# Kernel optimization log

Hardware: AMD Instinct MI355X
Metric: run time of the kernel (lower is better)

The kernel has to match this reference:

```python
import jax, jax.numpy as jnp
import numpy as np

B, T = 2, 4096
TOK_DIM, POS_DIM = 64, 64
N_HEADS, HEAD_DIM = 8, 32
D_MODEL = 256


def setup_inputs() -> dict:
    key = jax.random.key(0)
    ks = jax.random.split(key, 5)
    s = 0.02
    return {
        "x": jax.random.normal(ks[0], (B, T, TOK_DIM + POS_DIM), dtype=jnp.float32),
        "Wq": jax.random.normal(ks[1], (POS_DIM, N_HEADS * HEAD_DIM), dtype=jnp.float32) * s,
        "Wk": jax.random.normal(ks[2], (POS_DIM, N_HEADS * HEAD_DIM), dtype=jnp.float32) * s,
        "Wv": jax.random.normal(ks[3], (TOK_DIM, N_HEADS * HEAD_DIM), dtype=jnp.float32) * s,
        "Wo": jax.random.normal(ks[4], (N_HEADS * HEAD_DIM, D_MODEL), dtype=jnp.float32) * s,
    }


def reference(x, Wq, Wk, Wv, Wo):
    Bb, Tt, _ = x.shape
    x_tok = x[:, :, :TOK_DIM]   # V comes from token dims
    x_pos = x[:, :, TOK_DIM:]   # Q,K come from positional dims

    # [B, T, H, Dh] -> [B, H, T, Dh]
    q = (x_pos @ Wq).reshape(Bb, Tt, N_HEADS, HEAD_DIM).transpose(0, 2, 1, 3)
    k = (x_pos @ Wk).reshape(Bb, Tt, N_HEADS, HEAD_DIM).transpose(0, 2, 1, 3)
    v = (x_tok @ Wv).reshape(Bb, Tt, N_HEADS, HEAD_DIM).transpose(0, 2, 1, 3)

    scale = 1.0 / jnp.sqrt(jnp.float32(HEAD_DIM))
    scores = jnp.einsum("bhqd,bhkd->bhqk", q, k) * scale  # [B,H,T,T]
    causal = jnp.tril(jnp.ones((Tt, Tt), dtype=bool))
    scores = jnp.where(causal[None, None, :, :], scores, -jnp.inf)
    attn = jax.nn.softmax(scores, axis=-1)

    out = jnp.einsum("bhqk,bhkd->bhqd", attn, v)          # [B,H,T,Dh]
    out = out.transpose(0, 2, 1, 3).reshape(Bb, Tt, N_HEADS * HEAD_DIM)
    return out @ Wo
```

## Files before the change

### kernel.cpp

```cpp
#include <hip/hip_runtime.h>

typedef __attribute__((ext_vector_type(8))) short bf16x8;
typedef __attribute__((ext_vector_type(4))) float f32x4;
typedef __attribute__((ext_vector_type(16))) float f32x16;

#define NB 2
#define SEQ 4096
#define NHD 8
#define HDIM 32
#define DMODEL 256

#define QSCALE 0.25503506f

__device__ __forceinline__ short f2bf(float f) {
  union { float f; unsigned u; } v; v.f = f;
  unsigned r = v.u + 0x7fffu + ((v.u >> 16) & 1u);
  return (short)(r >> 16);
}

__global__ __launch_bounds__(256) void proj_kernel(
    const float* __restrict__ x, const float* __restrict__ Wq,
    const float* __restrict__ Wk, const float* __restrict__ Wv,
    short* __restrict__ Q, short* __restrict__ K, short* __restrict__ VT)
{
  __shared__ float xs[8][128];
  const int tid = threadIdx.x;
  const int row0 = blockIdx.x * 8;
  {
    const float4* src = (const float4*)(x + (size_t)row0 * 128);
    float4* dst = (float4*)xs;
    dst[tid] = src[tid];
  }
  __syncthreads();
  const int c = tid;
  float qa[8], ka[8], va[8];
#pragma unroll
  for (int r = 0; r < 8; ++r) { qa[r] = 0.f; ka[r] = 0.f; va[r] = 0.f; }
  for (int d4 = 0; d4 < 16; ++d4) {
    float wq[4], wk[4], wv[4];
#pragma unroll
    for (int j = 0; j < 4; ++j) {
      const int d = d4 * 4 + j;
      wq[j] = Wq[d * 256 + c];
      wk[j] = Wk[d * 256 + c];
      wv[j] = Wv[d * 256 + c];
    }
#pragma unroll
    for (int r = 0; r < 8; ++r) {
      const float4 xt = *(const float4*)&xs[r][d4 * 4];
      const float4 xp = *(const float4*)&xs[r][64 + d4 * 4];
      qa[r] += xp.x * wq[0] + xp.y * wq[1] + xp.z * wq[2] + xp.w * wq[3];
      ka[r] += xp.x * wk[0] + xp.y * wk[1] + xp.z * wk[2] + xp.w * wk[3];
      va[r] += xt.x * wv[0] + xt.y * wv[1] + xt.z * wv[2] + xt.w * wv[3];
    }
  }
  const int b = row0 >> 12;
  const int t0 = row0 & 4095;
  const int h = c >> 5, d = c & 31;
  const int bh = b * NHD + h;
#pragma unroll
  for (int r = 0; r < 8; ++r) {
    const int idx = (bh * SEQ + t0 + r) * HDIM + d;
    Q[idx] = f2bf(qa[r] * QSCALE);
    K[idx] = f2bf(ka[r]);
  }
  bf16x8 vv;
#pragma unroll
  for (int r = 0; r < 8; ++r) vv[r] = f2bf(va[r]);
  *(bf16x8*)&VT[(size_t)(bh * HDIM + d) * SEQ + t0] = vv;
}

__global__ __launch_bounds__(256) void wot_kernel(const float* __restrict__ Wo,
                                                  short* __restrict__ WoT)
{
  const int n = blockIdx.x;
  const int c = threadIdx.x;
  WoT[n * 256 + c] = f2bf(Wo[c * 256 + n]);
}

__global__ __launch_bounds__(256, 5) void attn_kernel(
    const short* __restrict__ Q, const short* __restrict__ K,
    const short* __restrict__ VT, short* __restrict__ O)
{
  __shared__ float MG[4][17][64];

  const int flat = blockIdx.x;
  const int bh = (flat & 7) + (((flat >> 3) & 1) << 3);
  const int tile = 127 - (flat >> 4);
  const int q0 = tile << 5;
  const int w = threadIdx.x >> 6;
  const int lane = threadIdx.x & 63;
  const int l31 = lane & 31;
  const int hi = lane >> 5;

  const short* Kb  = K  + (size_t)bh * SEQ * HDIM;
  const short* VTb = VT + (size_t)bh * HDIM * SEQ;

  const short* qrow = &Q[((size_t)bh * SEQ + q0 + l31) * HDIM + hi * 8];
  const bf16x8 qf0 = *(const bf16x8*)qrow;
  const bf16x8 qf1 = *(const bf16x8*)(qrow + 16);

  f32x16 acc = {0.f,0.f,0.f,0.f,0.f,0.f,0.f,0.f,0.f,0.f,0.f,0.f,0.f,0.f,0.f,0.f};
  const f32x16 z16 = {0.f,0.f,0.f,0.f,0.f,0.f,0.f,0.f,0.f,0.f,0.f,0.f,0.f,0.f,0.f,0.f};
  float lsum = 0.f;

  const int nc = tile + 1;
  for (int c = w; c < nc; c += 4) {
    const int kb = c << 5;
    const short* krow = &Kb[(size_t)(kb + l31) * HDIM + hi * 8];
    const bf16x8 kf0 = *(const bf16x8*)krow;
    const bf16x8 kf1 = *(const bf16x8*)(krow + 16);
    const short* vrow = &VTb[(size_t)l31 * SEQ + kb + hi * 8];
    const bf16x8 vf0 = *(const bf16x8*)vrow;
    const bf16x8 vf1 = *(const bf16x8*)(vrow + 16);

    f32x16 S = __builtin_amdgcn_mfma_f32_32x32x16_bf16(kf0, qf0, z16, 0, 0, 0);
    S = __builtin_amdgcn_mfma_f32_32x32x16_bf16(kf1, qf1, S, 0, 0, 0);

    unsigned Wd[8];
    if (kb == q0) {
#pragma unroll
      for (int i = 0; i < 8; ++i) {
        const int r0 = 2 * i;
        const int k0 = (r0 & 3) + ((r0 >> 2) << 3) + (hi << 2);
        float e0 = (k0     <= l31) ? __builtin_amdgcn_exp2f(S[r0])     : 0.f;
        float e1 = (k0 + 1 <= l31) ? __builtin_amdgcn_exp2f(S[r0 + 1]) : 0.f;
        lsum += e0 + e1;
        asm("v_cvt_pk_bf16_f32 %0, %1, %2" : "=v"(Wd[i]) : "v"(e0), "v"(e1));
      }
    } else {
#pragma unroll
      for (int i = 0; i < 8; ++i) {
        float e0 = __builtin_amdgcn_exp2f(S[2 * i]);
        float e1 = __builtin_amdgcn_exp2f(S[2 * i + 1]);
        lsum += e0 + e1;
        asm("v_cvt_pk_bf16_f32 %0, %1, %2" : "=v"(Wd[i]) : "v"(e0), "v"(e1));
      }
    }
    union { unsigned u[4]; bf16x8 v; } p0, p1;
    {
      unsigned s;
      s = __shfl_xor((int)Wd[2], 32); p0.u[0] = hi ? s : Wd[0];
      s = __shfl_xor((int)Wd[0], 32); p0.u[2] = hi ? Wd[2] : s;
      s = __shfl_xor((int)Wd[3], 32); p0.u[1] = hi ? s : Wd[1];
      s = __shfl_xor((int)Wd[1], 32); p0.u[3] = hi ? Wd[3] : s;
      s = __shfl_xor((int)Wd[6], 32); p1.u[0] = hi ? s : Wd[4];
      s = __shfl_xor((int)Wd[4], 32); p1.u[2] = hi ? Wd[6] : s;
      s = __shfl_xor((int)Wd[7], 32); p1.u[1] = hi ? s : Wd[5];
      s = __shfl_xor((int)Wd[5], 32); p1.u[3] = hi ? Wd[7] : s;
    }
    acc = __builtin_amdgcn_mfma_f32_32x32x16_bf16(vf0, p0.v, acc, 0, 0, 0);
    acc = __builtin_amdgcn_mfma_f32_32x32x16_bf16(vf1, p1.v, acc, 0, 0, 0);
  }

#pragma unroll
  for (int i = 0; i < 16; ++i) MG[w][i][lane] = acc[i];
  MG[w][16][lane] = lsum;
  __syncthreads();
  if (w == 0) {
    float fa[16];
#pragma unroll
    for (int i = 0; i < 16; ++i) fa[i] = 0.f;
    float fl = 0.f;
#pragma unroll
    for (int w2 = 0; w2 < 4; ++w2) {
#pragma unroll
      for (int i = 0; i < 16; ++i) fa[i] += MG[w2][i][lane];
      fl += MG[w2][16][lane] + MG[w2][16][lane ^ 32];
    }
    const float inv = 1.f / fl;
    const size_t obase = ((size_t)bh * SEQ + q0 + l31) * HDIM;
#pragma unroll
    for (int rg = 0; rg < 4; ++rg) {
      const int d0 = (rg << 3) + (hi << 2);
      short4 st;
      st.x = f2bf(fa[rg * 4 + 0] * inv);
      st.y = f2bf(fa[rg * 4 + 1] * inv);
      st.z = f2bf(fa[rg * 4 + 2] * inv);
      st.w = f2bf(fa[rg * 4 + 3] * inv);
      *(short4*)&O[obase + d0] = st;
    }
  }
}

__global__ __launch_bounds__(256) void ogemm_kernel(
    const short* __restrict__ O, const short* __restrict__ WoT, float* __restrict__ out)
{
  const int w = threadIdx.x >> 6;
  const int lane = threadIdx.x & 63;
  const int l15 = lane & 15, g = lane >> 4;
  const int m0 = blockIdx.x * 64 + w * 16;
  const int n0 = blockIdx.y * 64;
  const int b = m0 >> 12;
  const int t = (m0 & 4095) + l15;
  f32x4 acc[4];
#pragma unroll
  for (int i = 0; i < 4; ++i) acc[i] = (f32x4){0.f, 0.f, 0.f, 0.f};
#pragma unroll
  for (int ks = 0; ks < 8; ++ks) {
    const bf16x8 af = *(const bf16x8*)&O[(((size_t)b * NHD + ks) * SEQ + t) * HDIM + g * 8];
#pragma unroll
    for (int nt = 0; nt < 4; ++nt) {
      const bf16x8 bfr = *(const bf16x8*)&WoT[(n0 + nt * 16 + l15) * 256 + ks * 32 + g * 8];
      acc[nt] = __builtin_amdgcn_mfma_f32_16x16x32_bf16(af, bfr, acc[nt], 0, 0, 0);
    }
  }
#pragma unroll
  for (int nt = 0; nt < 4; ++nt)
#pragma unroll
    for (int r = 0; r < 4; ++r)
      out[(size_t)(m0 + (g << 2) + r) * 256 + n0 + nt * 16 + l15] = acc[nt][r];
}

extern "C" void kernel_launch(void* const* d_in, const int* in_sizes, int n_in,
                              void* d_out, int out_size, void* d_ws, size_t ws_size,
                              hipStream_t stream)
{
  const float* x  = (const float*)d_in[0];
  const float* Wq = (const float*)d_in[1];
  const float* Wk = (const float*)d_in[2];
  const float* Wv = (const float*)d_in[3];
  const float* Wo = (const float*)d_in[4];
  float* out = (float*)d_out;

  short* Q   = (short*)d_ws;
  short* K   = Q + 2097152;
  short* VT  = K + 2097152;
  short* O   = VT + 2097152;
  short* WoT = O + 2097152;

  proj_kernel<<<dim3(1024), dim3(256), 0, stream>>>(x, Wq, Wk, Wv, Q, K, VT);
  wot_kernel<<<dim3(256), dim3(256), 0, stream>>>(Wo, WoT);
  attn_kernel<<<dim3(2048), dim3(256), 0, stream>>>(Q, K, VT, O);
  ogemm_kernel<<<dim3(128, 4), dim3(256), 0, stream>>>(O, WoT, out);
}
```

Before: 147.9 us.

## Pair short and long causal query tiles per block, share K/V loads, prefetch

Measured after the change: 136.8 us. -7.5%, faster.

```diff
diff --git a/kernel.cpp b/kernel.cpp
--- a/kernel.cpp
+++ b/kernel.cpp
@@ -21,7 +21,9 @@
 __global__ __launch_bounds__(256) void proj_kernel(
     const float* __restrict__ x, const float* __restrict__ Wq,
     const float* __restrict__ Wk, const float* __restrict__ Wv,
-    short* __restrict__ Q, short* __restrict__ K, short* __restrict__ VT)
+    const float* __restrict__ Wo,
+    short* __restrict__ Q, short* __restrict__ K, short* __restrict__ VT,
+    short* __restrict__ WoT)
 {
   __shared__ float xs[8][128];
   const int tid = threadIdx.x;
@@ -31,6 +33,8 @@
     float4* dst = (float4*)xs;
     dst[tid] = src[tid];
   }
+  if (blockIdx.x < 256)
+    WoT[blockIdx.x * 256 + tid] = f2bf(Wo[tid * 256 + blockIdx.x]);
   __syncthreads();
   const int c = tid;
   float qa[8], ka[8], va[8];
@@ -70,24 +74,55 @@
   *(bf16x8*)&VT[(size_t)(bh * HDIM + d) * SEQ + t0] = vv;
 }
 
-__global__ __launch_bounds__(256) void wot_kernel(const float* __restrict__ Wo,
-                                                  short* __restrict__ WoT)
-{
-  const int n = blockIdx.x;
-  const int c = threadIdx.x;
-  WoT[n * 256 + c] = f2bf(Wo[c * 256 + n]);
-}
-
-__global__ __launch_bounds__(256, 5) void attn_kernel(
+__device__ __forceinline__ void score_to_p(const f32x16& S, bool masked, int hi, int l31,
+                                           float& lsum, bf16x8& p0v, bf16x8& p1v)
+{
+  unsigned Wd[8];
+  if (masked) {
+#pragma unroll
+    for (int i = 0; i < 8; ++i) {
+      const int r0 = 2 * i;
+      const int k0 = (r0 & 3) + ((r0 >> 2) << 3) + (hi << 2);
+      float e0 = (k0     <= l31) ? __builtin_amdgcn_exp2f(S[r0])     : 0.f;
+      float e1 = (k0 + 1 <= l31) ? __builtin_amdgcn_exp2f(S[r0 + 1]) : 0.f;
+      lsum += e0 + e1;
+      asm("v_cvt_pk_bf16_f32 %0, %1, %2" : "=v"(Wd[i]) : "v"(e0), "v"(e1));
+    }
+  } else {
+#pragma unroll
+    for (int i = 0; i < 8; ++i) {
+      float e0 = __builtin_amdgcn_exp2f(S[2 * i]);
+      float e1 = __builtin_amdgcn_exp2f(S[2 * i + 1]);
+      lsum += e0 + e1;
+      asm("v_cvt_pk_bf16_f32 %0, %1, %2" : "=v"(Wd[i]) : "v"(e0), "v"(e1));
+    }
+  }
+  union { unsigned u[4]; bf16x8 v; } p0, p1;
+  unsigned s;
+  s = __shfl_xor((int)Wd[2], 32); p0.u[0] = hi ? s : Wd[0];
+  s = __shfl_xor((int)Wd[0], 32); p0.u[2] = hi ? Wd[2] : s;
+  s = __shfl_xor((int)Wd[3], 32); p0.u[1] = hi ? s : Wd[1];
+  s = __shfl_xor((int)Wd[1], 32); p0.u[3] = hi ? Wd[3] : s;
+  s = __shfl_xor((int)Wd[6], 32); p1.u[0] = hi ? s : Wd[4];
+  s = __shfl_xor((int)Wd[4], 32); p1.u[2] = hi ? Wd[6] : s;
+  s = __shfl_xor((int)Wd[7], 32); p1.u[1] = hi ? s : Wd[5];
+  s = __shfl_xor((int)Wd[5], 32); p1.u[3] = hi ? Wd[7] : s;
+  p0v = p0.v; p1v = p1.v;
+}
+
+__global__ __launch_bounds__(256, 4) void attn_kernel(
     const short* __restrict__ Q, const short* __restrict__ K,
     const short* __restrict__ VT, short* __restrict__ O)
 {
-  __shared__ float MG[4][17][64];
+  __shared__ float MG[8][17][64];
 
   const int flat = blockIdx.x;
   const int bh = (flat & 7) + (((flat >> 3) & 1) << 3);
-  const int tile = 127 - (flat >> 4);
-  const int q0 = tile << 5;
+  const int p = flat >> 4;
+  const int tA = p, tB = 127 - p;
+  const int q0A = tA << 5, q0B = tB << 5;
+  const int ncA = tA + 1, ncB = tB + 1;
+
   const int w = threadIdx.x >> 6;
   const int lane = threadIdx.x & 63;
   const int l31 = lane & 31;
@@ -96,68 +131,70 @@
   const short* Kb  = K  + (size_t)bh * SEQ * HDIM;
   const short* VTb = VT + (size_t)bh * HDIM * SEQ;
 
-  const short* qrow = &Q[((size_t)bh * SEQ + q0 + l31) * HDIM + hi * 8];
-  const bf16x8 qf0 = *(const bf16x8*)qrow;
-  const bf16x8 qf1 = *(const bf16x8*)(qrow + 16);
-
-  f32x16 acc = {0.f,0.f,0.f,0.f,0.f,0.f,0.f,0.f,0.f,0.f,0.f,0.f,0.f,0.f,0.f,0.f};
+  const short* qrowA = &Q[((size_t)bh * SEQ + q0A + l31) * HDIM + hi * 8];
+  const bf16x8 qfA0 = *(const bf16x8*)qrowA;
+  const bf16x8 qfA1 = *(const bf16x8*)(qrowA + 16);
+  const short* qrowB = &Q[((size_t)bh * SEQ + q0B + l31) * HDIM + hi * 8];
+  const bf16x8 qfB0 = *(const bf16x8*)qrowB;
+  const bf16x8 qfB1 = *(const bf16x8*)(qrowB + 16);
+
   const f32x16 z16 = {0.f,0.f,0.f,0.f,0.f,0.f,0.f,0.f,0.f,0.f,0.f,0.f,0.f,0.f,0.f,0.f};
-  float lsum = 0.f;
-
-  const int nc = tile + 1;
-  for (int c = w; c < nc; c += 4) {
+  f32x16 accA = z16, accB = z16;
+  float lsumA = 0.f, lsumB = 0.f;
+
+  int c = w;
+  bf16x8 kf0, kf1, vf0, vf1;
+  if (c < ncB) {
     const int kb = c << 5;
     const short* krow = &Kb[(size_t)(kb + l31) * HDIM + hi * 8];
-    const bf16x8 kf0 = *(const bf16x8*)krow;
-    const bf16x8 kf1 = *(const bf16x8*)(krow + 16);
+    kf0 = *(const bf16x8*)krow;
+    kf1 = *(const bf16x8*)(krow + 16);
     const short* vrow = &VTb[(size_t)l31 * SEQ + kb + hi * 8];
-    const bf16x8 vf0 = *(const bf16x8*)vrow;
-    const bf16x8 vf1 = *(const bf16x8*)(vrow + 16);
-
-    f32x16 S = __builtin_amdgcn_mfma_f32_32x32x16_bf16(kf0, qf0, z16, 0, 0, 0);
-    S = __builtin_amdgcn_mfma_f32_32x32x16_bf16(kf1, qf1, S, 0, 0, 0);
-
-    unsigned Wd[8];
-    if (kb == q0) {
-#pragma unroll
-      for (int i = 0; i < 8; ++i) {
-        const int r0 = 2 * i;
-        const int k0 = (r0 & 3) + ((r0 >> 2) << 3) + (hi << 2);
-        float e0 = (k0     <= l31) ? __builtin_amdgcn_exp2f(S[r0])     : 0.f;
-        float e1 = (k0 + 1 <= l31) ? __builtin_amdgcn_exp2f(S[r0 + 1]) : 0.f;
-        lsum += e0 + e1;
-        asm("v_cvt_pk_bf16_f32 %0, %1, %2" : "=v"(Wd[i]) : "v"(e0), "v"(e1));
-      }
-    } else {
-#pragma unroll
-      for (int i = 0; i < 8; ++i) {
-        float e0 = __builtin_amdgcn_exp2f(S[2 * i]);
-        float e1 = __builtin_amdgcn_exp2f(S[2 * i + 1]);
-        lsum += e0 + e1;
-        asm("v_cvt_pk_bf16_f32 %0, %1, %2" : "=v"(Wd[i]) : "v"(e0), "v"(e1));
-      }
-    }
-    union { unsigned u[4]; bf16x8 v; } p0, p1;
+    vf0 = *(const bf16x8*)vrow;
+    vf1 = *(const bf16x8*)(vrow + 16);
+  }
+  for (; c < ncB; c += 4) {
+    const int kb = c << 5;
+    const int cn = c + 4;
+    bf16x8 kn0, kn1, vn0, vn1;
+    if (cn < ncB) {
+      const int kbn = cn << 5;
+      const short* krow = &Kb[(size_t)(kbn + l31) * HDIM + hi * 8];
+      kn0 = *(const bf16x8*)krow;
+      kn1 = *(const bf16x8*)(krow + 16);
+      const short* vrow = &VTb[(size_t)l31 * SEQ + kbn + hi * 8];
+      vn0 = *(const bf16x8*)vrow;
+      vn1 = *(const bf16x8*)(vrow + 16);
+    }
     {
-      unsigned s;
-      s = __shfl_xor((int)Wd[2], 32); p0.u[0] = hi ? s : Wd[0];
-      s = __shfl_xor((int)Wd[0], 32); p0.u[2] = hi ? Wd[2] : s;
-      s = __shfl_xor((int)Wd[3], 32); p0.u[1] = hi ? s : Wd[1];
-      s = __shfl_xor((int)Wd[1], 32); p0.u[3] = hi ? Wd[3] : s;
-      s = __shfl_xor((int)Wd[6], 32); p1.u[0] = hi ? s : Wd[4];
-      s = __shfl_xor((int)Wd[4], 32); p1.u[2] = hi ? Wd[6] : s;
-      s = __shfl_xor((int)Wd[7], 32); p1.u[1] = hi ? s : Wd[5];
-      s = __shfl_xor((int)Wd[5], 32); p1.u[3] = hi ? Wd[7] : s;
-    }
-    acc = __builtin_amdgcn_mfma_f32_32x32x16_bf16(vf0, p0.v, acc, 0, 0, 0);
-    acc = __builtin_amdgcn_mfma_f32_32x32x16_bf16(vf1, p1.v, acc, 0, 0, 0);
-  }
-
-#pragma unroll
-  for (int i = 0; i < 16; ++i) MG[w][i][lane] = acc[i];
-  MG[w][16][lane] = lsum;
+      f32x16 S = __builtin_amdgcn_mfma_f32_32x32x16_bf16(kf0, qfB0, z16, 0, 0, 0);
+      S = __builtin_amdgcn_mfma_f32_32x32x16_bf16(kf1, qfB1, S, 0, 0, 0);
+      bf16x8 p0v, p1v;
+      score_to_p(S, kb == q0B, hi, l31, lsumB, p0v, p1v);
+      accB = __builtin_amdgcn_mfma_f32_32x32x16_bf16(vf0, p0v, accB, 0, 0, 0);
+      accB = __builtin_amdgcn_mfma_f32_32x32x16_bf16(vf1, p1v, accB, 0, 0, 0);
+    }
+    if (c < ncA) {
+      f32x16 S = __builtin_amdgcn_mfma_f32_32x32x16_bf16(kf0, qfA0, z16, 0, 0, 0);
+      S = __builtin_amdgcn_mfma_f32_32x32x16_bf16(kf1, qfA1, S, 0, 0, 0);
+      bf16x8 p0v, p1v;
+      score_to_p(S, kb == q0A, hi, l31, lsumA, p0v, p1v);
+      accA = __builtin_amdgcn_mfma_f32_32x32x16_bf16(vf0, p0v, accA, 0, 0, 0);
+      accA = __builtin_amdgcn_mfma_f32_32x32x16_bf16(vf1, p1v, accA, 0, 0, 0);
+    }
+    kf0 = kn0; kf1 = kn1; vf0 = vn0; vf1 = vn1;
+  }
+
+#pragma unroll
+  for (int i = 0; i < 16; ++i) MG[w][i][lane] = accA[i];
+  MG[w][16][lane] = lsumA;
+#pragma unroll
+  for (int i = 0; i < 16; ++i) MG[4 + w][i][lane] = accB[i];
+  MG[4 + w][16][lane] = lsumB;
   __syncthreads();
-  if (w == 0) {
+  if (w < 2) {
+    const int base = w << 2;
+    const int q0 = w ? q0B : q0A;
     float fa[16];
 #pragma unroll
     for (int i = 0; i < 16; ++i) fa[i] = 0.f;
@@ -165,8 +202,8 @@
 #pragma unroll
     for (int w2 = 0; w2 < 4; ++w2) {
 #pragma unroll
-      for (int i = 0; i < 16; ++i) fa[i] += MG[w2][i][lane];
-      fl += MG[w2][16][lane] + MG[w2][16][lane ^ 32];
+      for (int i = 0; i < 16; ++i) fa[i] += MG[base + w2][i][lane];
+      fl += MG[base + w2][16][lane] + MG[base + w2][16][lane ^ 32];
     }
     const float inv = 1.f / fl;
     const size_t obase = ((size_t)bh * SEQ + q0 + l31) * HDIM;
@@ -229,8 +266,7 @@
   short* O   = VT + 2097152;
   short* WoT = O + 2097152;
 
-  proj_kernel<<<dim3(1024), dim3(256), 0, stream>>>(x, Wq, Wk, Wv, Q, K, VT);
-  wot_kernel<<<dim3(256), dim3(256), 0, stream>>>(Wo, WoT);
-  attn_kernel<<<dim3(2048), dim3(256), 0, stream>>>(Q, K, VT, O);
+  proj_kernel<<<dim3(1024), dim3(256), 0, stream>>>(x, Wq, Wk, Wv, Wo, Q, K, VT, WoT);
+  attn_kernel<<<dim3(1024), dim3(256), 0, stream>>>(Q, K, VT, O);
   ogemm_kernel<<<dim3(128, 4), dim3(256), 0, stream>>>(O, WoT, out);
 }
```
